# Kernel tuning notes

Measured on AMD Instinct MI355X. Metric: run time of the kernel, lower is better.

Reference implementation:

```python
import jax, jax.numpy as jnp
import numpy as np

EPS = 1e-7  # keras K.epsilon()
ROUTINGS = 3


def squash(v, axis=-1):
    s = jnp.sum(v * v, axis=axis, keepdims=True)
    scale = s / (1.0 + s) / jnp.sqrt(s + EPS)
    return scale * v


def setup_inputs() -> dict:
    key = jax.random.key(0)
    k1, k2 = jax.random.split(key)
    B, I, K = 256, 2048, 8   # batch, input_num_capsule, input_dim_capsule
    J, D = 10, 16            # num_capsule, dim_capsule
    inputs = jax.random.normal(k1, (B, I, K), dtype=jnp.float32)
    W = jax.random.normal(k2, (J, I, D, K), dtype=jnp.float32) * 0.05
    return {"inputs": inputs, "W": W}


def reference(inputs, W):
    # inputs: [B, I, K]; W: [J, I, D, K]
    # inputs_hat[b,j,i,d] = W[j,i] @ inputs[b,i]  -> [B, J, I, D]
    u_hat = jnp.einsum('jidk,bik->bjid', W, inputs)
    B, J, I, _ = u_hat.shape
    b = jnp.zeros((B, J, 1, I), dtype=u_hat.dtype)
    outputs = None
    for r in range(ROUTINGS):
        c = jax.nn.softmax(b, axis=1)                       # softmax over output capsules
        s = jnp.einsum('bjqi,bjid->bjqd', c, u_hat)          # [B, J, 1, D]
        outputs = squash(s, axis=-1)
        if r < ROUTINGS - 1:
            b = b + jnp.einsum('bjqd,bjid->bjqi', outputs, u_hat)
    return jnp.squeeze(outputs, axis=2)                      # [B, J, D]
```

## Files before the change

### kernel.cpp

```cpp
#include <hip/hip_runtime.h>
#include <math.h>


#define BB 256
#define II 2048
#define KK 8
#define JJ 10
#define DD 16

typedef __attribute__((ext_vector_type(4))) float f32x4;
typedef __attribute__((ext_vector_type(8))) short short8;

__device__ __forceinline__ short f2bf(float f) {
    union { float f; unsigned u; } v; v.f = f;
    unsigned r = v.u + 0x7FFFu + ((v.u >> 16) & 1u);
    return (short)(r >> 16);
}

__global__ __launch_bounds__(256) void cast_w_kernel(const float* __restrict__ W,
                                                     short* __restrict__ Wb) {
    const int idx = blockIdx.x * blockDim.x + threadIdx.x;
    const float4* src = (const float4*)(W + (size_t)idx * 8);
    const float4 a = src[0], b = src[1];
    short8 o;
    o[0] = f2bf(a.x); o[1] = f2bf(a.y); o[2] = f2bf(a.z); o[3] = f2bf(a.w);
    o[4] = f2bf(b.x); o[5] = f2bf(b.y); o[6] = f2bf(b.z); o[7] = f2bf(b.w);
    *(short8*)(Wb + (size_t)idx * 8) = o;
}

__global__ __launch_bounds__(256) void trans_x_kernel(const float* __restrict__ x,
                                                      short* __restrict__ xTb) {
    __shared__ float4 tile[8 * 66];
    const int t = threadIdx.x;
    const int b0 = blockIdx.y * 32, i0 = blockIdx.x * 8;
    {
        const int lb = t >> 3, li = t & 7;
        const float4* src = (const float4*)(x + ((b0 + lb) * II + (i0 + li)) * KK);
        tile[li * 66 + lb * 2 + 0] = src[0];
        tile[li * 66 + lb * 2 + 1] = src[1];
    }
    __syncthreads();
    {
        const int ri = t >> 5, rb = t & 31;
        const float4 p0 = tile[ri * 66 + rb * 2 + 0];
        const float4 p1 = tile[ri * 66 + rb * 2 + 1];
        short8 o;
        o[0] = f2bf(p0.x); o[1] = f2bf(p0.y); o[2] = f2bf(p0.z); o[3] = f2bf(p0.w);
        o[4] = f2bf(p1.x); o[5] = f2bf(p1.y); o[6] = f2bf(p1.z); o[7] = f2bf(p1.w);
        *(short8*)(xTb + ((size_t)(i0 + ri) * BB + (b0 + rb)) * KK) = o;
    }
}

#define LBUF 14336

__device__ __forceinline__ void seg_src_dst(int s, int i0, int b0,
                                            const short* __restrict__ xTb,
                                            const short* __restrict__ Wb,
                                            const short** src, int* dst) {
    if (s < 20) {
        const int j = s >> 1, h = s & 1;
        *src = Wb + ((size_t)(j * II + i0) * DD) * KK + h * 512;
        *dst = j * 1024 + h * 512;
    } else {
        const int il = s - 20;
        *src = xTb + ((size_t)(i0 + il) * BB + b0) * KK;
        *dst = 10240 + il * 512;
    }
}

template <int USE_C>
__global__ __launch_bounds__(256) void round_mfma(
    const short* __restrict__ xTb, const short* __restrict__ Wb,
    const float* __restrict__ vT, float* __restrict__ p)
{
    __shared__ short L[2][LBUF];
    const int t = threadIdx.x;
    const int lane = t & 63, wv = t >> 6;
    const int col = lane & 15, q = lane >> 4;
    const int b0 = blockIdx.y * 64;
    const int bl = wv * 16 + col;
    const int i0 = blockIdx.x * 16;

    short8 r0[7], r1[7];
#pragma unroll
    for (int n = 0; n < 7; ++n) {
        const int s = wv + n * 4;
        const short* src; int dst;
        seg_src_dst(s, i0, b0, xTb, Wb, &src, &dst);
        r0[n] = *(const short8*)(src + lane * 8);
        seg_src_dst(s, i0 + 8, b0, xTb, Wb, &src, &dst);
        r1[n] = *(const short8*)(src + lane * 8);
    }
#pragma unroll
    for (int n = 0; n < 7; ++n) {
        const int s = wv + n * 4;
        const short* src; int dst;
        seg_src_dst(s, i0, b0, xTb, Wb, &src, &dst);
        *(short8*)(&L[0][dst + lane * 8]) = r0[n];
    }
    __syncthreads();

    f32x4 sfrag[JJ];
#pragma unroll
    for (int j = 0; j < JJ; ++j) sfrag[j] = (f32x4){0.f, 0.f, 0.f, 0.f};

    float vfrag[JJ][4];
    if (USE_C) {
#pragma unroll
        for (int j = 0; j < JJ; ++j)
#pragma unroll
            for (int r = 0; r < 4; ++r)
                vfrag[j][r] = vT[(j * DD + q * 4 + r) * BB + b0 + bl];
    }

#pragma unroll
    for (int sc = 0; sc < 2; ++sc) {
        const short* Lb = L[sc];
        if (USE_C) {
            for (int il = 0; il < 8; ++il) {
                short8 A[JJ], Bf;
                const short8 z = (short8){0, 0, 0, 0, 0, 0, 0, 0};
                Bf = z;
#pragma unroll
                for (int j = 0; j < JJ; ++j) A[j] = z;
                if (q == 0) {
                    Bf = *(const short8*)(&Lb[10240 + il * 512 + bl * 8]);
#pragma unroll
                    for (int j = 0; j < JJ; ++j)
                        A[j] = *(const short8*)(&Lb[j * 1024 + il * 128 + col * 8]);
                }
                f32x4 U[JJ];
#pragma unroll
                for (int j = 0; j < JJ; ++j)
                    U[j] = __builtin_amdgcn_mfma_f32_16x16x32_bf16(
                        A[j], Bf, (f32x4){0.f, 0.f, 0.f, 0.f}, 0, 0, 0);
                float Lg[JJ];
#pragma unroll
                for (int j = 0; j < JJ; ++j)
                    Lg[j] = vfrag[j][0] * U[j][0] + vfrag[j][1] * U[j][1]
                          + vfrag[j][2] * U[j][2] + vfrag[j][3] * U[j][3];
#pragma unroll
                for (int j = 0; j < JJ; ++j) {
                    Lg[j] += __shfl_xor(Lg[j], 16, 64);
                    Lg[j] += __shfl_xor(Lg[j], 32, 64);
                }
                float sum = 0.f;
#pragma unroll
                for (int j = 0; j < JJ; ++j) { Lg[j] = __expf(Lg[j]); sum += Lg[j]; }
                const float inv = __builtin_amdgcn_rcpf(sum);
#pragma unroll
                for (int j = 0; j < JJ; ++j) {
                    const float c = Lg[j] * inv;
#pragma unroll
                    for (int r = 0; r < 4; ++r) sfrag[j][r] += c * U[j][r];
                }
            }
        } else {
#pragma unroll
            for (int s = 0; s < 2; ++s) {
                const int il = s * 4 + q;
                const short8 Bf = *(const short8*)(&Lb[10240 + il * 512 + bl * 8]);
#pragma unroll
                for (int j = 0; j < JJ; ++j) {
                    const short8 A = *(const short8*)(&Lb[j * 1024 + il * 128 + col * 8]);
                    sfrag[j] = __builtin_amdgcn_mfma_f32_16x16x32_bf16(A, Bf, sfrag[j], 0, 0, 0);
                }
            }
        }
        if (sc == 0) {
#pragma unroll
            for (int n = 0; n < 7; ++n) {
                const int s = wv + n * 4;
                const short* src; int dst;
                seg_src_dst(s, i0 + 8, b0, xTb, Wb, &src, &dst);
                *(short8*)(&L[1][dst + lane * 8]) = r1[n];
            }
            __syncthreads();
        }
    }

    float* pp = p + ((size_t)(blockIdx.y * 4 + wv) * 128 + blockIdx.x) * (JJ * 256);
#pragma unroll
    for (int j = 0; j < JJ; ++j)
        *(f32x4*)(pp + (j * 64 + lane) * 4) = sfrag[j];
}

template <int MODE>
__global__ __launch_bounds__(256) void rs_kernel(const float* __restrict__ p,
                                                 float* __restrict__ vT,
                                                 float* __restrict__ out, float scale) {
    __shared__ float red[256];
    __shared__ float cf[16];
    const int t = threadIdx.x;
    const int j = blockIdx.x, bt = blockIdx.y;
    const int d = t >> 4, bc = t & 15;
    const int lane = (d >> 2) * 16 + bc, r = d & 3;

    const float* pp = p + (size_t)bt * 128 * (JJ * 256) + j * 256 + lane * 4 + r;
    float sum = 0.f;
#pragma unroll 8
    for (int ch = 0; ch < 128; ++ch) sum += pp[(size_t)ch * (JJ * 256)];
    const float s = sum * scale;

    red[t] = s;
    __syncthreads();
    if (t < 16) {
        float ss = 0.f;
#pragma unroll
        for (int dd = 0; dd < DD; ++dd) {
            const float v = red[dd * 16 + t];
            ss += v * v;
        }
        cf[t] = ss / (1.f + ss) / sqrtf(ss + 1e-7f);
    }
    __syncthreads();
    const float v = cf[bc] * s;
    if (MODE == 0) vT[(j * DD + d) * BB + bt * 16 + bc] = v;
    if (MODE == 1) vT[(j * DD + d) * BB + bt * 16 + bc] += v;
    if (MODE == 2) out[((bt * 16 + bc) * JJ + j) * DD + d] = v;
}

#define IT_OLD 32
#define BT_OLD 16

__global__ __launch_bounds__(256) void zero_kernel(float* __restrict__ p, int n) {
    int idx = blockIdx.x * blockDim.x + threadIdx.x;
    if (idx < n) p[idx] = 0.f;
}

__global__ __launch_bounds__(256) void squash_old(float* __restrict__ s_acc,
                                                  float* __restrict__ dst, float scale,
                                                  int add_to_dst, int zero_src) {
    int idx = blockIdx.x * blockDim.x + threadIdx.x;
    if (idx >= BB * JJ) return;
    float s[DD];
    float ss = 0.f;
#pragma unroll
    for (int d = 0; d < DD; ++d) {
        s[d] = s_acc[idx * DD + d] * scale;
        ss += s[d] * s[d];
    }
    const float coef = ss / (1.f + ss) / sqrtf(ss + 1e-7f);
#pragma unroll
    for (int d = 0; d < DD; ++d) {
        const float vv = coef * s[d];
        if (add_to_dst) dst[idx * DD + d] += vv;
        else            dst[idx * DD + d] = vv;
        if (zero_src)   s_acc[idx * DD + d] = 0.f;
    }
}

__global__ __launch_bounds__(256) void round1_old(const float* __restrict__ x,
                                                  const float* __restrict__ W,
                                                  float* __restrict__ s_acc) {
    const int t = threadIdx.x;
    const int d = t & 15;
    const int bq = t >> 4;
    const int b = blockIdx.y * BT_OLD + bq;
    const int i0 = blockIdx.x * IT_OLD;
    float acc[JJ];
#pragma unroll
    for (int j = 0; j < JJ; ++j) acc[j] = 0.f;
    for (int ii = 0; ii < IT_OLD; ++ii) {
        const int i = i0 + ii;
        const float* xp = x + ((b * II) + i) * KK;
        const float4 xa = *(const float4*)(xp);
        const float4 xb = *(const float4*)(xp + 4);
#pragma unroll
        for (int j = 0; j < JJ; ++j) {
            const float* wp = W + (((j * II + i) * DD + d) * KK);
            const float4 w0 = *(const float4*)(wp);
            const float4 w1 = *(const float4*)(wp + 4);
            acc[j] += w0.x*xa.x + w0.y*xa.y + w0.z*xa.z + w0.w*xa.w
                    + w1.x*xb.x + w1.y*xb.y + w1.z*xb.z + w1.w*xb.w;
        }
    }
#pragma unroll
    for (int j = 0; j < JJ; ++j)
        atomicAdd(&s_acc[(b * JJ + j) * DD + d], acc[j]);
}

__global__ __launch_bounds__(256) void round_old(const float* __restrict__ x,
                                                 const float* __restrict__ W,
                                                 const float* __restrict__ v,
                                                 float* __restrict__ s_acc) {
    const int t = threadIdx.x;
    const int d = t & 15;
    const int bq = t >> 4;
    const int b = blockIdx.y * BT_OLD + bq;
    const int i0 = blockIdx.x * IT_OLD;
    float vr[JJ], acc[JJ];
#pragma unroll
    for (int j = 0; j < JJ; ++j) {
        vr[j] = v[(b * JJ + j) * DD + d];
        acc[j] = 0.f;
    }
    for (int ii = 0; ii < IT_OLD; ++ii) {
        const int i = i0 + ii;
        const float* xp = x + ((b * II) + i) * KK;
        const float4 xa = *(const float4*)(xp);
        const float4 xb = *(const float4*)(xp + 4);
        float U[JJ], Lg[JJ];
#pragma unroll
        for (int j = 0; j < JJ; ++j) {
            const float* wp = W + (((j * II + i) * DD + d) * KK);
            const float4 w0 = *(const float4*)(wp);
            const float4 w1 = *(const float4*)(wp + 4);
            U[j] = w0.x*xa.x + w0.y*xa.y + w0.z*xa.z + w0.w*xa.w
                 + w1.x*xb.x + w1.y*xb.y + w1.z*xb.z + w1.w*xb.w;
            Lg[j] = vr[j] * U[j];
        }
#pragma unroll
        for (int m = 8; m >= 1; m >>= 1) {
#pragma unroll
            for (int j = 0; j < JJ; ++j) Lg[j] += __shfl_xor(Lg[j], m, 64);
        }
        float mx = Lg[0];
#pragma unroll
        for (int j = 1; j < JJ; ++j) mx = fmaxf(mx, Lg[j]);
        float sum = 0.f;
#pragma unroll
        for (int j = 0; j < JJ; ++j) { Lg[j] = __expf(Lg[j] - mx); sum += Lg[j]; }
        const float inv = 1.f / sum;
#pragma unroll
        for (int j = 0; j < JJ; ++j) acc[j] += (Lg[j] * inv) * U[j];
    }
#pragma unroll
    for (int j = 0; j < JJ; ++j)
        atomicAdd(&s_acc[(b * JJ + j) * DD + d], acc[j]);
}

extern "C" void kernel_launch(void* const* d_in, const int* in_sizes, int n_in,
                              void* d_out, int out_size, void* d_ws, size_t ws_size,
                              hipStream_t stream) {
    const float* x = (const float*)d_in[0];
    const float* W = (const float*)d_in[1];
    float* out = (float*)d_out;

    float* vT  = (float*)d_ws;
    float* p   = vT + BB * JJ * DD;
    short* xTb = (short*)(p + (size_t)16 * 128 * 2560);
    short* Wb  = xTb + (size_t)II * BB * KK;
    const size_t need = (size_t)(BB * JJ * DD + 16 * 128 * 2560) * 4
                      + ((size_t)II * BB * KK + (size_t)JJ * II * DD * KK) * 2;

    if (ws_size >= need) {
        cast_w_kernel<<<(JJ * II * DD * KK / 8) / 256, 256, 0, stream>>>(W, Wb);
        trans_x_kernel<<<dim3(II / 8, BB / 32), 256, 0, stream>>>(x, xTb);

        dim3 rg(128, 4);
        dim3 sg(JJ, 16);
        round_mfma<0><<<rg, 256, 0, stream>>>(xTb, Wb, vT, p);
        rs_kernel<0><<<sg, 256, 0, stream>>>(p, vT, out, 0.1f);
        round_mfma<1><<<rg, 256, 0, stream>>>(xTb, Wb, vT, p);
        rs_kernel<1><<<sg, 256, 0, stream>>>(p, vT, out, 1.0f);
        round_mfma<1><<<rg, 256, 0, stream>>>(xTb, Wb, vT, p);
        rs_kernel<2><<<sg, 256, 0, stream>>>(p, vT, out, 1.0f);
    } else {
        float* s_acc = (float*)d_ws;
        float* v_buf = s_acc + BB * JJ * DD;
        const int NS = BB * JJ * DD;
        dim3 rg(II / IT_OLD, BB / BT_OLD);
        zero_kernel<<<(NS + 255) / 256, 256, 0, stream>>>(s_acc, NS);
        round1_old<<<rg, 256, 0, stream>>>(x, W, s_acc);
        squash_old<<<(BB * JJ + 255) / 256, 256, 0, stream>>>(s_acc, v_buf, 0.1f, 0, 1);
        round_old<<<rg, 256, 0, stream>>>(x, W, v_buf, s_acc);
        squash_old<<<(BB * JJ + 255) / 256, 256, 0, stream>>>(s_acc, v_buf, 1.0f, 1, 1);
        round_old<<<rg, 256, 0, stream>>>(x, W, v_buf, s_acc);
        squash_old<<<(BB * JJ + 255) / 256, 256, 0, stream>>>(s_acc, out, 1.0f, 0, 0);
    }
}
```

Before: 163.7 us.

## Store partial sums in fp16, merge prep kernels, restructure reduce kernel

The MFMA round kernel now writes its per-block partial sums as fp16 instead of fp32, which halves the partial buffer traffic read by the reduction kernel. The reduction kernel is restructured so each thread reads four packed halves across a quarter of the chunks, then combines through shared memory and computes the squash norm with wave shuffles. The W cast and x transpose kernels are merged into one launch to save a launch. fp16 partials lose precision and could overflow on larger values.

```diff
diff --git a/kernel.cpp b/kernel.cpp
--- a/kernel.cpp
+++ b/kernel.cpp
@@ -17,37 +17,40 @@
     return (short)(r >> 16);
 }
 
-__global__ __launch_bounds__(256) void cast_w_kernel(const float* __restrict__ W,
-                                                     short* __restrict__ Wb) {
-    const int idx = blockIdx.x * blockDim.x + threadIdx.x;
-    const float4* src = (const float4*)(W + (size_t)idx * 8);
-    const float4 a = src[0], b = src[1];
-    short8 o;
-    o[0] = f2bf(a.x); o[1] = f2bf(a.y); o[2] = f2bf(a.z); o[3] = f2bf(a.w);
-    o[4] = f2bf(b.x); o[5] = f2bf(b.y); o[6] = f2bf(b.z); o[7] = f2bf(b.w);
-    *(short8*)(Wb + (size_t)idx * 8) = o;
-}
-
-__global__ __launch_bounds__(256) void trans_x_kernel(const float* __restrict__ x,
-                                                      short* __restrict__ xTb) {
+__global__ __launch_bounds__(256) void pre_kernel(const float* __restrict__ x,
+                                                  const float* __restrict__ W,
+                                                  short* __restrict__ xTb,
+                                                  short* __restrict__ Wb) {
     __shared__ float4 tile[8 * 66];
     const int t = threadIdx.x;
-    const int b0 = blockIdx.y * 32, i0 = blockIdx.x * 8;
-    {
-        const int lb = t >> 3, li = t & 7;
-        const float4* src = (const float4*)(x + ((b0 + lb) * II + (i0 + li)) * KK);
-        tile[li * 66 + lb * 2 + 0] = src[0];
-        tile[li * 66 + lb * 2 + 1] = src[1];
-    }
-    __syncthreads();
-    {
-        const int ri = t >> 5, rb = t & 31;
-        const float4 p0 = tile[ri * 66 + rb * 2 + 0];
-        const float4 p1 = tile[ri * 66 + rb * 2 + 1];
+    const int bid = blockIdx.x;
+    if (bid < 1280) {
+        const int idx = bid * 256 + t;
+        const float4* src = (const float4*)(W + (size_t)idx * 8);
+        const float4 a = src[0], b = src[1];
         short8 o;
-        o[0] = f2bf(p0.x); o[1] = f2bf(p0.y); o[2] = f2bf(p0.z); o[3] = f2bf(p0.w);
-        o[4] = f2bf(p1.x); o[5] = f2bf(p1.y); o[6] = f2bf(p1.z); o[7] = f2bf(p1.w);
-        *(short8*)(xTb + ((size_t)(i0 + ri) * BB + (b0 + rb)) * KK) = o;
+        o[0] = f2bf(a.x); o[1] = f2bf(a.y); o[2] = f2bf(a.z); o[3] = f2bf(a.w);
+        o[4] = f2bf(b.x); o[5] = f2bf(b.y); o[6] = f2bf(b.z); o[7] = f2bf(b.w);
+        *(short8*)(Wb + (size_t)idx * 8) = o;
+    } else {
+        const int bb = bid - 1280;
+        const int b0 = (bb >> 8) * 32, i0 = (bb & 255) * 8;
+        {
+            const int lb = t >> 3, li = t & 7;
+            const float4* src = (const float4*)(x + ((b0 + lb) * II + (i0 + li)) * KK);
+            tile[li * 66 + lb * 2 + 0] = src[0];
+            tile[li * 66 + lb * 2 + 1] = src[1];
+        }
+        __syncthreads();
+        {
+            const int ri = t >> 5, rb = t & 31;
+            const float4 p0 = tile[ri * 66 + rb * 2 + 0];
+            const float4 p1 = tile[ri * 66 + rb * 2 + 1];
+            short8 o;
+            o[0] = f2bf(p0.x); o[1] = f2bf(p0.y); o[2] = f2bf(p0.z); o[3] = f2bf(p0.w);
+            o[4] = f2bf(p1.x); o[5] = f2bf(p1.y); o[6] = f2bf(p1.z); o[7] = f2bf(p1.w);
+            *(short8*)(xTb + ((size_t)(i0 + ri) * BB + (b0 + rb)) * KK) = o;
+        }
     }
 }
 
@@ -71,7 +74,7 @@
 template <int USE_C>
 __global__ __launch_bounds__(256) void round_mfma(
     const short* __restrict__ xTb, const short* __restrict__ Wb,
-    const float* __restrict__ vT, float* __restrict__ p)
+    const float* __restrict__ vT, _Float16* __restrict__ p)
 {
     __shared__ short L[2][LBUF];
     const int t = threadIdx.x;
@@ -179,45 +182,57 @@
         }
     }
 
-    float* pp = p + ((size_t)(blockIdx.y * 4 + wv) * 128 + blockIdx.x) * (JJ * 256);
-#pragma unroll
-    for (int j = 0; j < JJ; ++j)
-        *(f32x4*)(pp + (j * 64 + lane) * 4) = sfrag[j];
+    _Float16* pp = p + ((size_t)(blockIdx.y * 4 + wv) * 128 + blockIdx.x) * (JJ * 256);
+#pragma unroll
+    for (int j = 0; j < JJ; ++j) {
+        union { uint2 u; _Float16 h[4]; } pk;
+        pk.h[0] = (_Float16)sfrag[j][0];
+        pk.h[1] = (_Float16)sfrag[j][1];
+        pk.h[2] = (_Float16)sfrag[j][2];
+        pk.h[3] = (_Float16)sfrag[j][3];
+        *(uint2*)(pp + (size_t)(j * 64 + lane) * 4) = pk.u;
+    }
 }
 
 template <int MODE>
-__global__ __launch_bounds__(256) void rs_kernel(const float* __restrict__ p,
+__global__ __launch_bounds__(256) void rs_kernel(const _Float16* __restrict__ p,
                                                  float* __restrict__ vT,
                                                  float* __restrict__ out, float scale) {
-    __shared__ float red[256];
-    __shared__ float cf[16];
+    __shared__ f32x4 red[256];
     const int t = threadIdx.x;
     const int j = blockIdx.x, bt = blockIdx.y;
-    const int d = t >> 4, bc = t & 15;
-    const int lane = (d >> 2) * 16 + bc, r = d & 3;
-
-    const float* pp = p + (size_t)bt * 128 * (JJ * 256) + j * 256 + lane * 4 + r;
-    float sum = 0.f;
+    const int eg = t & 63, cg = t >> 6;
+
+    const _Float16* pp = p + ((size_t)bt * 128 + cg * 32) * (JJ * 256) + j * 256 + eg * 4;
+    float s0 = 0.f, s1 = 0.f, s2 = 0.f, s3 = 0.f;
 #pragma unroll 8
-    for (int ch = 0; ch < 128; ++ch) sum += pp[(size_t)ch * (JJ * 256)];
-    const float s = sum * scale;
-
-    red[t] = s;
+    for (int ch = 0; ch < 32; ++ch) {
+        union { uint2 u; _Float16 h[4]; } cv;
+        cv.u = *(const uint2*)(pp + (size_t)ch * (JJ * 256));
+        s0 += (float)cv.h[0]; s1 += (float)cv.h[1];
+        s2 += (float)cv.h[2]; s3 += (float)cv.h[3];
+    }
+    red[t] = (f32x4){s0, s1, s2, s3};
     __syncthreads();
-    if (t < 16) {
-        float ss = 0.f;
-#pragma unroll
-        for (int dd = 0; dd < DD; ++dd) {
-            const float v = red[dd * 16 + t];
-            ss += v * v;
-        }
-        cf[t] = ss / (1.f + ss) / sqrtf(ss + 1e-7f);
-    }
-    __syncthreads();
-    const float v = cf[bc] * s;
-    if (MODE == 0) vT[(j * DD + d) * BB + bt * 16 + bc] = v;
-    if (MODE == 1) vT[(j * DD + d) * BB + bt * 16 + bc] += v;
-    if (MODE == 2) out[((bt * 16 + bc) * JJ + j) * DD + d] = v;
+    if (t < 64) {
+        f32x4 a = red[t];
+        a += red[64 + t]; a += red[128 + t]; a += red[192 + t];
+        const float x0 = a[0] * scale, x1 = a[1] * scale;
+        const float x2 = a[2] * scale, x3 = a[3] * scale;
+        float ss = x0 * x0 + x1 * x1 + x2 * x2 + x3 * x3;
+        ss += __shfl_xor(ss, 16, 64);
+        ss += __shfl_xor(ss, 32, 64);
+        const float coef = ss / (1.f + ss) / sqrtf(ss + 1e-7f);
+        const int qd = t >> 4, bc = t & 15;
+        const float v[4] = {coef * x0, coef * x1, coef * x2, coef * x3};
+#pragma unroll
+        for (int r = 0; r < 4; ++r) {
+            const int d = qd * 4 + r;
+            if (MODE == 0) vT[(j * DD + d) * BB + bt * 16 + bc] = v[r];
+            if (MODE == 1) vT[(j * DD + d) * BB + bt * 16 + bc] += v[r];
+            if (MODE == 2) out[((bt * 16 + bc) * JJ + j) * DD + d] = v[r];
+        }
+    }
 }
 
 #define IT_OLD 32
@@ -337,16 +352,16 @@
     const float* W = (const float*)d_in[1];
     float* out = (float*)d_out;
 
-    float* vT  = (float*)d_ws;
-    float* p   = vT + BB * JJ * DD;
-    short* xTb = (short*)(p + (size_t)16 * 128 * 2560);
-    short* Wb  = xTb + (size_t)II * BB * KK;
-    const size_t need = (size_t)(BB * JJ * DD + 16 * 128 * 2560) * 4
+    float* vT     = (float*)d_ws;
+    _Float16* p   = (_Float16*)(vT + BB * JJ * DD);
+    short* xTb    = (short*)(p + (size_t)16 * 128 * 2560);
+    short* Wb     = xTb + (size_t)II * BB * KK;
+    const size_t need = (size_t)(BB * JJ * DD) * 4
+                      + (size_t)16 * 128 * 2560 * 2
                       + ((size_t)II * BB * KK + (size_t)JJ * II * DD * KK) * 2;
 
     if (ws_size >= need) {
-        cast_w_kernel<<<(JJ * II * DD * KK / 8) / 256, 256, 0, stream>>>(W, Wb);
-        trans_x_kernel<<<dim3(II / 8, BB / 32), 256, 0, stream>>>(x, xTb);
+        pre_kernel<<<1280 + 2048, 256, 0, stream>>>(x, W, xTb, Wb);
 
         dim3 rg(128, 4);
         dim3 sg(JJ, 16);
```

New measurement: 139.9 us. 14.5% less time.
